# Kernel tuning notes

Hardware: AMD Instinct MI355X
Metric: run time of the kernel (lower is better)

The kernel has to match this reference:

```python
import jax, jax.numpy as jnp
import numpy as np

# Winograd F(4x4, 3x3) transform matrices (m=4, r=3, a=6)
B_T = jnp.array([[4.,0.,-5.,0.,1.,0.],
                 [0.,-4.,-4.,1.,1.,0.],
                 [0.,4.,-4.,-1.,1.,0.],
                 [0.,-2.,-1.,2.,1.,0.],
                 [0.,2.,-1.,-2.,1.,0.],
                 [0.,4.,0.,-5.,0.,1.]], dtype=jnp.float32)
G = jnp.array([[1/4.,0.,0.],
               [-1/6.,-1/6.,-1/6.],
               [-1/6.,1/6.,-1/6.],
               [1/24.,1/12.,1/6.],
               [1/24.,-1/12.,1/6.],
               [0.,0.,1.]], dtype=jnp.float32)
A_T = jnp.array([[1.,1.,1.,1.,1.,0.],
                 [0.,1.,-1.,2.,-2.,0.],
                 [0.,1.,1.,4.,4.,0.],
                 [0.,1.,-1.,8.,-8.,1.]], dtype=jnp.float32)

M_OUT, R_K, A_IN = 4, 3, 6  # output tile m, kernel r, input tile a = m+r-1


def setup_inputs() -> dict:
    key = jax.random.key(0)
    k1, k2 = jax.random.split(key)
    x = jax.random.normal(k1, (16, 64, 130, 130), dtype=jnp.float32)
    w = jax.random.normal(k2, (64, 64, 3, 3), dtype=jnp.float32) * 0.05
    return {"input": x, "weight": w}


def reference(input, weight):
    N, C, H, W = input.shape
    K = weight.shape[0]
    m, r, a = M_OUT, R_K, A_IN
    T = (H - r + 1) // m  # tiles per spatial dim (perfect tiling)

    # Filter transform: U[k,c] = G @ w[k,c] @ G^T  -> [K,C,a,a]
    U = jnp.einsum('ai,kcij,bj->kcab', G, weight, G)

    # Extract overlapping a x a input tiles with stride m: [N,C,T,a,T,a]
    idx = (jnp.arange(T) * m)[:, None] + jnp.arange(a)[None, :]  # [T,a]
    tiles = input[:, :, idx, :][:, :, :, :, idx]

    # Input transform: V = B^T @ tile @ B  -> [N,T,T,C,a,a]
    V = jnp.einsum('ai,nctisj,bj->ntscab', B_T, tiles, B_T)
    Vp = V.reshape(N * T * T, C, a, a)  # [P,C,a,a]

    # Elementwise (tile-domain) multiply + channel reduce: M[p,k] = sum_c U[k,c]*V[p,c]
    Mt = jnp.einsum('kcab,pcab->pkab', U, Vp)  # [P,K,a,a]

    # Output transform: Y_tile = A^T @ M @ A -> [P,K,m,m]
    Yt = jnp.einsum('ai,pkij,bj->pkab', A_T, Mt, A_T)

    out = T * m  # = H - r + 1
    Y = Yt.reshape(N, T, T, K, m, m).transpose(0, 3, 1, 4, 2, 5).reshape(N, K, out, out)
    return Y
```

## Files before the change

kernel.cpp:

```cpp
#include <hip/hip_runtime.h>


__constant__ float c_AT[24] = {
  1.f, 0.f, 0.f, 0.f,
  1.f, 1.f, 1.f, 1.f,
  1.f,-1.f, 1.f,-1.f,
  1.f, 2.f, 4.f, 8.f,
  1.f,-2.f, 4.f,-8.f,
  0.f, 0.f, 0.f, 1.f
};

__device__ __forceinline__ void gl2lds16(const float* g, float* l) {
  __builtin_amdgcn_global_load_lds((const __attribute__((address_space(1))) void*)g,
                                   (__attribute__((address_space(3))) void*)l, 16, 0, 0);
}

__global__ __launch_bounds__(256) void k_filter(const float* __restrict__ w,
                                                float* __restrict__ U) {
  int g = blockIdx.x * 256 + threadIdx.x;
  int k = g & 63;
  int c = g >> 6;
  const float* wp = w + (size_t)(k * 64 + c) * 9;
  float w00 = wp[0], w01 = wp[1], w02 = wp[2];
  float w10 = wp[3], w11 = wp[4], w12 = wp[5];
  float w20 = wp[6], w21 = wp[7], w22 = wp[8];
  const float G[6][3] = {
    {0.25f, 0.f, 0.f},
    {-1.f/6.f, -1.f/6.f, -1.f/6.f},
    {-1.f/6.f,  1.f/6.f, -1.f/6.f},
    {1.f/24.f,  1.f/12.f, 1.f/6.f},
    {1.f/24.f, -1.f/12.f, 1.f/6.f},
    {0.f, 0.f, 1.f}
  };
  float t[6][3];
#pragma unroll
  for (int a = 0; a < 6; ++a) {
    t[a][0] = G[a][0]*w00 + G[a][1]*w10 + G[a][2]*w20;
    t[a][1] = G[a][0]*w01 + G[a][1]*w11 + G[a][2]*w21;
    t[a][2] = G[a][0]*w02 + G[a][1]*w12 + G[a][2]*w22;
  }
#pragma unroll
  for (int a = 0; a < 6; ++a) {
#pragma unroll
    for (int b = 0; b < 6; ++b) {
      float u = G[b][0]*t[a][0] + G[b][1]*t[a][1] + G[b][2]*t[a][2];
      U[(size_t)(a*6+b)*4096 + c*64 + k] = u;
    }
  }
}

__global__ __launch_bounds__(256) void k_input(const float* __restrict__ x,
                                               float* __restrict__ V,
                                               int n0, int Pchunk) {
  __shared__ float Ls[34*134];
  const int tid  = threadIdx.x;
  const int bi   = blockIdx.x;
  const int band = bi & 3;
  const int c    = (bi >> 2) & 63;
  const int nl   = bi >> 8;
  const float* xp = x + (size_t)((n0 + nl) * 64 + c) * (130*130) + band * 32 * 130;
  for (int idx = tid; idx < 34*65; idx += 256) {
    int r  = idx / 65;
    int c2 = idx - r * 65;
    *(float2*)&Ls[r*134 + c2*2] = *(const float2*)(xp + r*130 + c2*2);
  }
  __syncthreads();
  const int tyl = tid >> 5;
  const int tx  = tid & 31;
  const int ty  = band * 8 + tyl;
  const int p   = (nl * 32 + ty) * 32 + tx;
  const float* bl = &Ls[(tyl*4)*134 + tx*4];
  float t1[6][6];
#pragma unroll
  for (int j = 0; j < 6; ++j) {
    float d0 = bl[0*134+j], d1 = bl[1*134+j], d2 = bl[2*134+j];
    float d3 = bl[3*134+j], d4 = bl[4*134+j], d5 = bl[5*134+j];
    t1[0][j] =  4.f*d0 - 5.f*d2 + d4;
    t1[1][j] = -4.f*d1 - 4.f*d2 + d3 + d4;
    t1[2][j] =  4.f*d1 - 4.f*d2 - d3 + d4;
    t1[3][j] = -2.f*d1 -     d2 + 2.f*d3 + d4;
    t1[4][j] =  2.f*d1 -     d2 - 2.f*d3 + d4;
    t1[5][j] =  4.f*d1 - 5.f*d3 + d5;
  }
  float* vb = V + (size_t)c * Pchunk + p;
  const size_t abs_ = (size_t)64 * Pchunk;
#pragma unroll
  for (int a = 0; a < 6; ++a) {
    float s0=t1[a][0], s1=t1[a][1], s2=t1[a][2], s3=t1[a][3], s4=t1[a][4], s5=t1[a][5];
    float v0 =  4.f*s0 - 5.f*s2 + s4;
    float v1 = -4.f*s1 - 4.f*s2 + s3 + s4;
    float v2 =  4.f*s1 - 4.f*s2 - s3 + s4;
    float v3 = -2.f*s1 -     s2 + 2.f*s3 + s4;
    float v4 =  2.f*s1 -     s2 - 2.f*s3 + s4;
    float v5 =  4.f*s1 - 5.f*s3 + s5;
    vb[(size_t)(a*6+0)*abs_] = v0;
    vb[(size_t)(a*6+1)*abs_] = v1;
    vb[(size_t)(a*6+2)*abs_] = v2;
    vb[(size_t)(a*6+3)*abs_] = v3;
    vb[(size_t)(a*6+4)*abs_] = v4;
    vb[(size_t)(a*6+5)*abs_] = v5;
  }
}

__global__ __launch_bounds__(256, 2) void k_gemm3(const float* __restrict__ V,
                                                  const float* __restrict__ U,
                                                  float* __restrict__ M,
                                                  int Pchunk, int nPB) {
  __shared__ float Vs[2][16][512];
  const int tid  = threadIdx.x;
  const int lane = tid & 63;
  const int wv   = tid >> 6;
  const unsigned bx = blockIdx.x;
  const int ab = bx / (unsigned)nPB;
  const int pb = bx - ab * nPB;
  const int p0 = pb * 512;
  const float* Vab = V + (size_t)ab * 64 * Pchunk + p0;
  const float* Uab = U + (size_t)ab * 4096;
  const int k0 = __builtin_amdgcn_readfirstlane(wv * 16);

#define STAGE(cc, buf)                                                        \
  {                                                                           \
    _Pragma("unroll")                                                         \
    for (int i = 0; i < 8; ++i) {                                             \
      int h = wv * 8 + i;                                                     \
      int r = h >> 1, hf = h & 1;                                             \
      gl2lds16(Vab + (size_t)((cc)*16 + r) * Pchunk + hf*256 + lane*4,        \
               &Vs[(buf)][r][hf*256]);                                        \
    }                                                                         \
  }

  float acc[16][8];
#pragma unroll
  for (int kk = 0; kk < 16; ++kk)
#pragma unroll
    for (int pp = 0; pp < 8; ++pp) acc[kk][pp] = 0.f;

  STAGE(0, 0);
  for (int cc = 0; cc < 4; ++cc) {
    __syncthreads();
    if (cc < 3) STAGE(cc + 1, (cc + 1) & 1);
    const float* vsb = &Vs[cc & 1][0][0];
#pragma unroll
    for (int c = 0; c < 16; ++c) {
      const float* uc = Uab + (size_t)(cc * 16 + c) * 64 + k0;
      float4 va = *(const float4*)(vsb + c * 512 + lane * 4);
      float4 vb = *(const float4*)(vsb + c * 512 + 256 + lane * 4);
      float vv[8] = {va.x, va.y, va.z, va.w, vb.x, vb.y, vb.z, vb.w};
#pragma unroll
      for (int kk = 0; kk < 16; ++kk) {
        float u = uc[kk];
#pragma unroll
        for (int pp = 0; pp < 8; ++pp) acc[kk][pp] += u * vv[pp];
      }
    }
  }
#undef STAGE

  float* mb = M + ((size_t)ab * 64 + k0) * Pchunk + p0;
#pragma unroll
  for (int kk = 0; kk < 16; ++kk) {
    *(float4*)(mb + (size_t)kk * Pchunk + lane * 4) =
        make_float4(acc[kk][0], acc[kk][1], acc[kk][2], acc[kk][3]);
    *(float4*)(mb + (size_t)kk * Pchunk + 256 + lane * 4) =
        make_float4(acc[kk][4], acc[kk][5], acc[kk][6], acc[kk][7]);
  }
}

__global__ __launch_bounds__(256) void k_out2(const float* __restrict__ M,
                                              float* __restrict__ out,
                                              int n0, int Pchunk, int bpk) {
  const unsigned bx = blockIdx.x;
  const int k    = bx / (unsigned)bpk;
  const int pblk = bx - k * bpk;
  const int p    = pblk * 1024 + threadIdx.x * 4;
  const int nl = p >> 10;
  const int ty = (p >> 5) & 31;
  const int tx = p & 31;

  const float* mp = M + (size_t)k * Pchunk + p;
  const size_t abstride = (size_t)64 * Pchunk;

  float Y[4][4][4];
#pragma unroll
  for (int u = 0; u < 4; ++u)
#pragma unroll
    for (int v = 0; v < 4; ++v)
#pragma unroll
      for (int q = 0; q < 4; ++q) Y[u][v][q] = 0.f;

#pragma unroll
  for (int i = 0; i < 6; ++i) {
    float R[4][4];
#pragma unroll
    for (int v = 0; v < 4; ++v)
#pragma unroll
      for (int q = 0; q < 4; ++q) R[v][q] = 0.f;
#pragma unroll
    for (int j = 0; j < 6; ++j) {
      float4 m4 = *(const float4*)(mp + (size_t)(i * 6 + j) * abstride);
      float mm[4] = {m4.x, m4.y, m4.z, m4.w};
#pragma unroll
      for (int v = 0; v < 4; ++v) {
        float av = c_AT[j * 4 + v];
#pragma unroll
        for (int q = 0; q < 4; ++q) R[v][q] += av * mm[q];
      }
    }
#pragma unroll
    for (int u = 0; u < 4; ++u) {
      float au = c_AT[i * 4 + u];
#pragma unroll
      for (int v = 0; v < 4; ++v)
#pragma unroll
        for (int q = 0; q < 4; ++q) Y[u][v][q] += au * R[v][q];
    }
  }

  float* ob = out + ((size_t)((n0 + nl) * 64 + k) * 128 + ty * 4) * 128 + tx * 4;
#pragma unroll
  for (int u = 0; u < 4; ++u)
    *(float4*)(ob + (size_t)u * 128) = make_float4(Y[u][0][0], Y[u][1][0], Y[u][2][0], Y[u][3][0])
    , *(float4*)(ob + (size_t)u * 128 + 4)  = make_float4(Y[u][0][1], Y[u][1][1], Y[u][2][1], Y[u][3][1])
    , *(float4*)(ob + (size_t)u * 128 + 8)  = make_float4(Y[u][0][2], Y[u][1][2], Y[u][2][2], Y[u][3][2])
    , *(float4*)(ob + (size_t)u * 128 + 12) = make_float4(Y[u][0][3], Y[u][1][3], Y[u][2][3], Y[u][3][3]);
}

extern "C" void kernel_launch(void* const* d_in, const int* in_sizes, int n_in,
                              void* d_out, int out_size, void* d_ws, size_t ws_size,
                              hipStream_t stream) {
  const float* x = (const float*)d_in[0];
  const float* w = (const float*)d_in[1];
  float* out = (float*)d_out;
  float* U = (float*)d_ws;
  const size_t U_bytes = 36ull * 64 * 64 * 4;
  const size_t per_n = 2ull * 36 * 1024 * 64 * 4;
  size_t avail = ws_size > U_bytes ? ws_size - U_bytes : 0;
  int chunk = (int)(avail / per_n);
  if (chunk < 1) return;
  if (chunk > 8) chunk = 8;

  k_filter<<<16, 256, 0, stream>>>(w, U);
  for (int n0 = 0; n0 < 16; n0 += chunk) {
    int cn = (16 - n0) < chunk ? (16 - n0) : chunk;
    int Pchunk = cn * 1024;
    float* V = (float*)((char*)d_ws + U_bytes);
    float* M = V + (size_t)36 * 64 * Pchunk;
    int nPBg = cn * 2;
    k_input<<<cn*256,   256, 0, stream>>>(x, V, n0, Pchunk);
    k_gemm3<<<36*nPBg,  256, 0, stream>>>(V, U, M, Pchunk, nPBg);
    k_out2 <<<64*cn,    256, 0, stream>>>(M, out, n0, Pchunk, cn);
  }
}
```

Baseline: 298.4 us.

## Use split-fp16 MFMA for Winograd batched GEMM with channel-minor V layout

Replaces the fp32 FMA batched GEMM with MFMA 32x32x16 f16 instructions. Each operand is split into high and low fp16 halves, packed in one 32-bit word, and three MFMA products are summed to keep near-fp32 accuracy. The input and filter transforms now write packed hi/lo values in a channel-minor layout, using an LDS staging buffer for the V transpose and an XOR-swizzled LDS load in the GEMM. This moves the GEMM onto the matrix cores at the cost of three MFMAs per product, extra pack and permute work, and a more complex input-transform kernel.

After: 429.8 us. +44.0%, slower.

```diff
diff --git a/kernel.cpp b/kernel.cpp
--- a/kernel.cpp
+++ b/kernel.cpp
@@ -1,5 +1,9 @@
 #include <hip/hip_runtime.h>
-
+#include <hip/hip_fp16.h>
+
+
+typedef _Float16 half8_t __attribute__((ext_vector_type(8)));
+typedef float floatx16 __attribute__((ext_vector_type(16)));
 
 __constant__ float c_AT[24] = {
   1.f, 0.f, 0.f, 0.f,
@@ -10,16 +14,25 @@
   0.f, 0.f, 0.f, 1.f
 };
 
-__device__ __forceinline__ void gl2lds16(const float* g, float* l) {
-  __builtin_amdgcn_global_load_lds((const __attribute__((address_space(1))) void*)g,
-                                   (__attribute__((address_space(3))) void*)l, 16, 0, 0);
-}
+__device__ __forceinline__ uint32_t pack_hilo(float v) {
+  __half hh = __float2half(v);
+  float r = v - __half2float(hh);
+  __half hl = __float2half(r);
+  return (uint32_t)__half_as_ushort(hh) | ((uint32_t)__half_as_ushort(hl) << 16);
+}
+__device__ __forceinline__ uint32_t phi(uint32_t w0, uint32_t w1) {
+  return __builtin_amdgcn_perm(w1, w0, 0x05040100u);
+}
+__device__ __forceinline__ uint32_t plo(uint32_t w0, uint32_t w1) {
+  return __builtin_amdgcn_perm(w1, w0, 0x07060302u);
+}
+union H8 { uint32_t u[4]; half8_t h; };
 
 __global__ __launch_bounds__(256) void k_filter(const float* __restrict__ w,
-                                                float* __restrict__ U) {
+                                                uint32_t* __restrict__ U) {
   int g = blockIdx.x * 256 + threadIdx.x;
-  int k = g & 63;
-  int c = g >> 6;
+  int c = g & 63;
+  int k = g >> 6;
   const float* wp = w + (size_t)(k * 64 + c) * 9;
   float w00 = wp[0], w01 = wp[1], w02 = wp[2];
   float w10 = wp[3], w11 = wp[4], w12 = wp[5];
@@ -44,125 +57,156 @@
 #pragma unroll
     for (int b = 0; b < 6; ++b) {
       float u = G[b][0]*t[a][0] + G[b][1]*t[a][1] + G[b][2]*t[a][2];
-      U[(size_t)(a*6+b)*4096 + c*64 + k] = u;
+      U[((size_t)(a*6+b)*64 + k)*64 + c] = pack_hilo(u);
     }
   }
 }
 
 __global__ __launch_bounds__(256) void k_input(const float* __restrict__ x,
-                                               float* __restrict__ V,
+                                               uint32_t* __restrict__ V,
                                                int n0, int Pchunk) {
-  __shared__ float Ls[34*134];
-  const int tid  = threadIdx.x;
-  const int bi   = blockIdx.x;
-  const int band = bi & 3;
-  const int c    = (bi >> 2) & 63;
-  const int nl   = bi >> 8;
-  const float* xp = x + (size_t)((n0 + nl) * 64 + c) * (130*130) + band * 32 * 130;
-  for (int idx = tid; idx < 34*65; idx += 256) {
-    int r  = idx / 65;
-    int c2 = idx - r * 65;
-    *(float2*)&Ls[r*134 + c2*2] = *(const float2*)(xp + r*130 + c2*2);
-  }
-  __syncthreads();
-  const int tyl = tid >> 5;
-  const int tx  = tid & 31;
-  const int ty  = band * 8 + tyl;
-  const int p   = (nl * 32 + ty) * 32 + tx;
-  const float* bl = &Ls[(tyl*4)*134 + tx*4];
-  float t1[6][6];
-#pragma unroll
-  for (int j = 0; j < 6; ++j) {
-    float d0 = bl[0*134+j], d1 = bl[1*134+j], d2 = bl[2*134+j];
-    float d3 = bl[3*134+j], d4 = bl[4*134+j], d5 = bl[5*134+j];
-    t1[0][j] =  4.f*d0 - 5.f*d2 + d4;
-    t1[1][j] = -4.f*d1 - 4.f*d2 + d3 + d4;
-    t1[2][j] =  4.f*d1 - 4.f*d2 - d3 + d4;
-    t1[3][j] = -2.f*d1 -     d2 + 2.f*d3 + d4;
-    t1[4][j] =  2.f*d1 -     d2 - 2.f*d3 + d4;
-    t1[5][j] =  4.f*d1 - 5.f*d3 + d5;
-  }
-  float* vb = V + (size_t)c * Pchunk + p;
-  const size_t abs_ = (size_t)64 * Pchunk;
-#pragma unroll
-  for (int a = 0; a < 6; ++a) {
-    float s0=t1[a][0], s1=t1[a][1], s2=t1[a][2], s3=t1[a][3], s4=t1[a][4], s5=t1[a][5];
-    float v0 =  4.f*s0 - 5.f*s2 + s4;
-    float v1 = -4.f*s1 - 4.f*s2 + s3 + s4;
-    float v2 =  4.f*s1 - 4.f*s2 - s3 + s4;
-    float v3 = -2.f*s1 -     s2 + 2.f*s3 + s4;
-    float v4 =  2.f*s1 -     s2 - 2.f*s3 + s4;
-    float v5 =  4.f*s1 - 5.f*s3 + s5;
-    vb[(size_t)(a*6+0)*abs_] = v0;
-    vb[(size_t)(a*6+1)*abs_] = v1;
-    vb[(size_t)(a*6+2)*abs_] = v2;
-    vb[(size_t)(a*6+3)*abs_] = v3;
-    vb[(size_t)(a*6+4)*abs_] = v4;
-    vb[(size_t)(a*6+5)*abs_] = v5;
-  }
-}
-
-__global__ __launch_bounds__(256, 2) void k_gemm3(const float* __restrict__ V,
-                                                  const float* __restrict__ U,
-                                                  float* __restrict__ M,
-                                                  int Pchunk, int nPB) {
-  __shared__ float Vs[2][16][512];
+  __shared__ float XL[4*1330];
+  __shared__ uint32_t VL[36*64*4];
+  const int tid = threadIdx.x;
+  const int bi  = blockIdx.x;
+  const int cg  = bi & 3;
+  const int ty2 = (bi >> 2) & 15;
+  const int nl  = bi >> 6;
+  const int h0  = ty2 * 8;
+
+  const int c4 = tid & 3;
+  const int p  = tid >> 2;
+  const int trow = p >> 5, pl = p & 31;
+
+  for (int ch = 0; ch < 4; ++ch) {
+    const int cbase = cg*16 + ch*4;
+    __syncthreads();
+    for (int idx = tid; idx < 4*10*65; idx += 256) {
+      int cc = idx / 650; int rem = idx - cc*650; int r = rem/65; int j = rem - r*65;
+      const float* xr = x + ((size_t)((n0+nl)*64 + cbase + cc)*130 + h0 + r)*130;
+      float2 v = *(const float2*)(xr + j*2);
+      XL[cc*1330 + r*133 + j*2]     = v.x;
+      XL[cc*1330 + r*133 + j*2 + 1] = v.y;
+    }
+    __syncthreads();
+    const float* bl = &XL[c4*1330 + (trow*4)*133 + pl*4];
+    float t1[6][6];
+#pragma unroll
+    for (int j = 0; j < 6; ++j) {
+      float d0 = bl[0*133+j], d1 = bl[1*133+j], d2 = bl[2*133+j];
+      float d3 = bl[3*133+j], d4 = bl[4*133+j], d5 = bl[5*133+j];
+      t1[0][j] =  4.f*d0 - 5.f*d2 + d4;
+      t1[1][j] = -4.f*d1 - 4.f*d2 + d3 + d4;
+      t1[2][j] =  4.f*d1 - 4.f*d2 - d3 + d4;
+      t1[3][j] = -2.f*d1 -     d2 + 2.f*d3 + d4;
+      t1[4][j] =  2.f*d1 -     d2 - 2.f*d3 + d4;
+      t1[5][j] =  4.f*d1 - 5.f*d3 + d5;
+    }
+#pragma unroll
+    for (int a = 0; a < 6; ++a) {
+      float s0=t1[a][0], s1=t1[a][1], s2=t1[a][2], s3=t1[a][3], s4=t1[a][4], s5=t1[a][5];
+      float v0 =  4.f*s0 - 5.f*s2 + s4;
+      float v1 = -4.f*s1 - 4.f*s2 + s3 + s4;
+      float v2 =  4.f*s1 - 4.f*s2 - s3 + s4;
+      float v3 = -2.f*s1 -     s2 + 2.f*s3 + s4;
+      float v4 =  2.f*s1 -     s2 - 2.f*s3 + s4;
+      float v5 =  4.f*s1 - 5.f*s3 + s5;
+      VL[(a*6+0)*256 + p*4 + c4] = pack_hilo(v0);
+      VL[(a*6+1)*256 + p*4 + c4] = pack_hilo(v1);
+      VL[(a*6+2)*256 + p*4 + c4] = pack_hilo(v2);
+      VL[(a*6+3)*256 + p*4 + c4] = pack_hilo(v3);
+      VL[(a*6+4)*256 + p*4 + c4] = pack_hilo(v4);
+      VL[(a*6+5)*256 + p*4 + c4] = pack_hilo(v5);
+    }
+    __syncthreads();
+#pragma unroll
+    for (int i = 0; i < 9; ++i) {
+      int e = i*256 + tid; int ab = e >> 6; int pp = e & 63;
+      uint4 q = *(const uint4*)&VL[ab*256 + pp*4];
+      size_t pglob = (size_t)nl*1024 + ty2*64 + pp;
+      *(uint4*)&V[((size_t)ab*Pchunk + pglob)*64 + cbase] = q;
+    }
+  }
+}
+
+__global__ __launch_bounds__(256) void k_gemm(const uint32_t* __restrict__ V,
+                                              const uint32_t* __restrict__ U,
+                                              float* __restrict__ M,
+                                              int Pchunk, int nPB) {
+  __shared__ uint32_t Vs[128*64];
   const int tid  = threadIdx.x;
   const int lane = tid & 63;
   const int wv   = tid >> 6;
   const unsigned bx = blockIdx.x;
   const int ab = bx / (unsigned)nPB;
   const int pb = bx - ab * nPB;
-  const int p0 = pb * 512;
-  const float* Vab = V + (size_t)ab * 64 * Pchunk + p0;
-  const float* Uab = U + (size_t)ab * 4096;
-  const int k0 = __builtin_amdgcn_readfirstlane(wv * 16);
-
-#define STAGE(cc, buf)                                                        \
-  {                                                                           \
-    _Pragma("unroll")                                                         \
-    for (int i = 0; i < 8; ++i) {                                             \
-      int h = wv * 8 + i;                                                     \
-      int r = h >> 1, hf = h & 1;                                             \
-      gl2lds16(Vab + (size_t)((cc)*16 + r) * Pchunk + hf*256 + lane*4,        \
-               &Vs[(buf)][r][hf*256]);                                        \
-    }                                                                         \
-  }
-
-  float acc[16][8];
-#pragma unroll
-  for (int kk = 0; kk < 16; ++kk)
-#pragma unroll
-    for (int pp = 0; pp < 8; ++pp) acc[kk][pp] = 0.f;
-
-  STAGE(0, 0);
+  const int p0 = pb * 128;
+
+  const uint4* Vg = (const uint4*)(V + ((size_t)ab*Pchunk + p0)*64);
+  uint4 tmp[8];
+#pragma unroll
+  for (int i = 0; i < 8; ++i) tmp[i] = Vg[tid + i*256];
+#pragma unroll
+  for (int i = 0; i < 8; ++i) {
+    int f = tid + i*256; int pp = f >> 4; int u = f & 15;
+    *(uint4*)&Vs[pp*64 + (u ^ (pp & 15))*4] = tmp[i];
+  }
+  __syncthreads();
+
+  const int kg = lane >> 5;
+  const int m  = lane & 31;
+  half8_t Uhi[2][4], Ulo[2][4];
+#pragma unroll
+  for (int t = 0; t < 2; ++t) {
+    int k = t*32 + m;
+    const uint32_t* ub = U + ((size_t)ab*64 + k)*64;
+#pragma unroll
+    for (int cc = 0; cc < 4; ++cc) {
+      uint4 qa = *(const uint4*)(ub + cc*16 + kg*8);
+      uint4 qb = *(const uint4*)(ub + cc*16 + kg*8 + 4);
+      H8 hi, lo;
+      hi.u[0] = phi(qa.x, qa.y); hi.u[1] = phi(qa.z, qa.w);
+      hi.u[2] = phi(qb.x, qb.y); hi.u[3] = phi(qb.z, qb.w);
+      lo.u[0] = plo(qa.x, qa.y); lo.u[1] = plo(qa.z, qa.w);
+      lo.u[2] = plo(qb.x, qb.y); lo.u[3] = plo(qb.z, qb.w);
+      Uhi[t][cc] = hi.h; Ulo[t][cc] = lo.h;
+    }
+  }
+
+  floatx16 acc[2];
+#pragma unroll
+  for (int t = 0; t < 2; ++t)
+#pragma unroll
+    for (int r = 0; r < 16; ++r) acc[t][r] = 0.f;
+
+  const int plane = wv*32 + m;
+#pragma unroll
   for (int cc = 0; cc < 4; ++cc) {
-    __syncthreads();
-    if (cc < 3) STAGE(cc + 1, (cc + 1) & 1);
-    const float* vsb = &Vs[cc & 1][0][0];
-#pragma unroll
-    for (int c = 0; c < 16; ++c) {
-      const float* uc = Uab + (size_t)(cc * 16 + c) * 64 + k0;
-      float4 va = *(const float4*)(vsb + c * 512 + lane * 4);
-      float4 vb = *(const float4*)(vsb + c * 512 + 256 + lane * 4);
-      float vv[8] = {va.x, va.y, va.z, va.w, vb.x, vb.y, vb.z, vb.w};
-#pragma unroll
-      for (int kk = 0; kk < 16; ++kk) {
-        float u = uc[kk];
-#pragma unroll
-        for (int pp = 0; pp < 8; ++pp) acc[kk][pp] += u * vv[pp];
-      }
-    }
-  }
-#undef STAGE
-
-  float* mb = M + ((size_t)ab * 64 + k0) * Pchunk + p0;
-#pragma unroll
-  for (int kk = 0; kk < 16; ++kk) {
-    *(float4*)(mb + (size_t)kk * Pchunk + lane * 4) =
-        make_float4(acc[kk][0], acc[kk][1], acc[kk][2], acc[kk][3]);
-    *(float4*)(mb + (size_t)kk * Pchunk + 256 + lane * 4) =
-        make_float4(acc[kk][4], acc[kk][5], acc[kk][6], acc[kk][7]);
+    int u0 = (cc*4 + kg*2) ^ (plane & 15);
+    int u1 = (cc*4 + kg*2 + 1) ^ (plane & 15);
+    uint4 qa = *(const uint4*)&Vs[plane*64 + u0*4];
+    uint4 qb = *(const uint4*)&Vs[plane*64 + u1*4];
+    H8 vhi, vlo;
+    vhi.u[0] = phi(qa.x, qa.y); vhi.u[1] = phi(qa.z, qa.w);
+    vhi.u[2] = phi(qb.x, qb.y); vhi.u[3] = phi(qb.z, qb.w);
+    vlo.u[0] = plo(qa.x, qa.y); vlo.u[1] = plo(qa.z, qa.w);
+    vlo.u[2] = plo(qb.x, qb.y); vlo.u[3] = plo(qb.z, qb.w);
+#pragma unroll
+    for (int t = 0; t < 2; ++t) {
+      acc[t] = __builtin_amdgcn_mfma_f32_32x32x16_f16(Uhi[t][cc], vhi.h, acc[t], 0, 0, 0);
+      acc[t] = __builtin_amdgcn_mfma_f32_32x32x16_f16(Uhi[t][cc], vlo.h, acc[t], 0, 0, 0);
+      acc[t] = __builtin_amdgcn_mfma_f32_32x32x16_f16(Ulo[t][cc], vhi.h, acc[t], 0, 0, 0);
+    }
+  }
+
+  const int pout = p0 + wv*32 + m;
+#pragma unroll
+  for (int t = 0; t < 2; ++t) {
+#pragma unroll
+    for (int r = 0; r < 16; ++r) {
+      int k = t*32 + (r & 3) + 8*(r >> 2) + 4*kg;
+      M[((size_t)ab*64 + k)*Pchunk + pout] = acc[t][r];
+    }
   }
 }
 
@@ -218,11 +262,12 @@
 
   float* ob = out + ((size_t)((n0 + nl) * 64 + k) * 128 + ty * 4) * 128 + tx * 4;
 #pragma unroll
-  for (int u = 0; u < 4; ++u)
-    *(float4*)(ob + (size_t)u * 128) = make_float4(Y[u][0][0], Y[u][1][0], Y[u][2][0], Y[u][3][0])
-    , *(float4*)(ob + (size_t)u * 128 + 4)  = make_float4(Y[u][0][1], Y[u][1][1], Y[u][2][1], Y[u][3][1])
-    , *(float4*)(ob + (size_t)u * 128 + 8)  = make_float4(Y[u][0][2], Y[u][1][2], Y[u][2][2], Y[u][3][2])
-    , *(float4*)(ob + (size_t)u * 128 + 12) = make_float4(Y[u][0][3], Y[u][1][3], Y[u][2][3], Y[u][3][3]);
+  for (int u = 0; u < 4; ++u) {
+    *(float4*)(ob + (size_t)u * 128)      = make_float4(Y[u][0][0], Y[u][1][0], Y[u][2][0], Y[u][3][0]);
+    *(float4*)(ob + (size_t)u * 128 + 4)  = make_float4(Y[u][0][1], Y[u][1][1], Y[u][2][1], Y[u][3][1]);
+    *(float4*)(ob + (size_t)u * 128 + 8)  = make_float4(Y[u][0][2], Y[u][1][2], Y[u][2][2], Y[u][3][2]);
+    *(float4*)(ob + (size_t)u * 128 + 12) = make_float4(Y[u][0][3], Y[u][1][3], Y[u][2][3], Y[u][3][3]);
+  }
 }
 
 extern "C" void kernel_launch(void* const* d_in, const int* in_sizes, int n_in,
@@ -231,7 +276,7 @@
   const float* x = (const float*)d_in[0];
   const float* w = (const float*)d_in[1];
   float* out = (float*)d_out;
-  float* U = (float*)d_ws;
+  uint32_t* U = (uint32_t*)d_ws;
   const size_t U_bytes = 36ull * 64 * 64 * 4;
   const size_t per_n = 2ull * 36 * 1024 * 64 * 4;
   size_t avail = ws_size > U_bytes ? ws_size - U_bytes : 0;
@@ -243,11 +288,11 @@
   for (int n0 = 0; n0 < 16; n0 += chunk) {
     int cn = (16 - n0) < chunk ? (16 - n0) : chunk;
     int Pchunk = cn * 1024;
-    float* V = (float*)((char*)d_ws + U_bytes);
-    float* M = V + (size_t)36 * 64 * Pchunk;
-    int nPBg = cn * 2;
-    k_input<<<cn*256,   256, 0, stream>>>(x, V, n0, Pchunk);
-    k_gemm3<<<36*nPBg,  256, 0, stream>>>(V, U, M, Pchunk, nPBg);
-    k_out2 <<<64*cn,    256, 0, stream>>>(M, out, n0, Pchunk, cn);
-  }
-}
+    uint32_t* V = (uint32_t*)((char*)d_ws + U_bytes);
+    float* M = (float*)(V + (size_t)36 * Pchunk * 64);
+    int nPB = Pchunk / 128;
+    k_input<<<cn*64,  256, 0, stream>>>(x, V, n0, Pchunk);
+    k_gemm <<<36*nPB, 256, 0, stream>>>(V, U, M, Pchunk, nPB);
+    k_out2 <<<64*cn,  256, 0, stream>>>(M, out, n0, Pchunk, cn);
+  }
+}
```
